# Performance work log

Measured on AMD Instinct MI355X. Metric: run time of the kernel, lower is better.

Reference implementation:

```python
import jax, jax.numpy as jnp
import numpy as np

REEIG_EPS = 1e-4  # SPDNet ReEig eigenvalue floor


def _semi_orth(key, ni, no):
    a = jax.random.normal(key, (ni, no), dtype=jnp.float32)
    q, _ = jnp.linalg.qr(a)  # columns orthonormal (ni >= no)
    return q[None]  # (1, ni, no)


def setup_inputs() -> dict:
    key = jax.random.key(0)
    ks = jax.random.split(key, 6)
    N, C, T, V = 256, 256, 64, 25
    x = jax.random.normal(ks[0], (N, C, T, V), dtype=jnp.float32)
    W1 = _semi_orth(ks[1], 25, 20)
    W2 = _semi_orth(ks[2], 20, 15)
    W3 = _semi_orth(ks[3], 15, 10)
    fc_w = jax.random.normal(ks[4], (64, 100), dtype=jnp.float32) * (1.0 / np.sqrt(100))
    fc_b = jax.random.normal(ks[5], (64,), dtype=jnp.float32) * 0.01
    return {"x": x, "W1": W1, "W2": W2, "W3": W3, "fc_w": fc_w, "fc_b": fc_b}


def _bimap(X, W):
    # X: (n, h, ni, ni), W: (h, ni, no) -> W^T X W : (n, h, no, no)
    return jnp.einsum('hji,nhjk,hkl->nhil', W, X, W)


def _reeig(X):
    w, u = jnp.linalg.eigh(X)
    w = jnp.maximum(w, REEIG_EPS)
    return jnp.einsum('...ij,...j,...kj->...ik', u, w, u)


def _logeig(X):
    w, u = jnp.linalg.eigh(X)
    return jnp.einsum('...ij,...j,...kj->...ik', u, jnp.log(w), u)


def reference(x, W1, W2, W3, fc_w, fc_b):
    N, C, T, V = x.shape
    xm = x.mean(axis=2)                      # (N, C, V): mean over time
    d = xm - xm.mean(axis=1, keepdims=True)  # center over channel samples
    cov = jnp.einsum('ncv,ncw->nvw', d, d) / (C - 1)  # (N, V, V), fused reduction
    cov = cov + jnp.float32(1e-8) * jnp.eye(V, dtype=x.dtype)
    X = cov[:, None, :, :]                   # (N, 1, V, V)
    X = _reeig(_bimap(X, W1))                # 25 -> 20
    X = _reeig(_bimap(X, W2))                # 20 -> 15
    X = _logeig(_reeig(_bimap(X, W3)))       # 15 -> 10, matrix log
    feat = X.reshape(N, -1)                  # (N, 100)
    return feat @ fc_w.T + fc_b              # (N, 64)
```

## Files before the change

kernel.cpp:

```cpp
#include <hip/hip_runtime.h>
#include <math.h>


__device__ __constant__ int d_pairs[9][5][2] = {
    {{9,0},{1,8},{2,7},{3,6},{4,5}},
    {{9,1},{2,0},{3,8},{4,7},{5,6}},
    {{9,2},{3,1},{4,0},{5,8},{6,7}},
    {{9,3},{4,2},{5,1},{6,0},{7,8}},
    {{9,4},{5,3},{6,2},{7,1},{8,0}},
    {{9,5},{6,4},{7,3},{8,2},{0,1}},
    {{9,6},{7,5},{8,4},{0,3},{1,2}},
    {{9,7},{8,6},{0,5},{1,4},{2,3}},
    {{9,8},{0,7},{1,6},{2,5},{3,4}},
};

__global__ __launch_bounds__(1024) void topo_kernel(
    const float* __restrict__ x,
    const float* __restrict__ W1,
    const float* __restrict__ W2,
    const float* __restrict__ W3,
    const float* __restrict__ fcw,
    const float* __restrict__ fcb,
    float* __restrict__ out)
{
    __shared__ float s_xm[6400];
    __shared__ float s_mean[32];
    __shared__ float s_w1[500];
    __shared__ float s_w2[300];
    __shared__ float s_w3[152];
    __shared__ float s_t1[375];
    __shared__ float s_wc[250];
    __shared__ float s_E[2560];
    __shared__ float s_A[100];
    __shared__ float s_U[100];
    __shared__ float s_cp[10], s_cq[10];
    __shared__ int   s_ip[10], s_iq[10];
    __shared__ float s_lw[16];
    __shared__ float s_Y[100];
    __shared__ float s_fcw[100 * 65];

    const int tid = threadIdx.x;
    const int n = blockIdx.x;
    const float* xb = x + (size_t)n * (256 * 64 * 25);

    for (int g = tid; g < 6400; g += 1024) {
        int o = g / 100, k = g - o * 100;
        s_fcw[k * 65 + o] = fcw[g];
    }
    for (int g = tid; g < 500; g += 1024) s_w1[g] = W1[g];
    for (int g = tid; g < 300; g += 1024) s_w2[g] = W2[g];
    if (tid < 150) s_w3[tid] = W3[tid];
    for (int g = tid; g < 6400; g += 1024) s_xm[g] = 0.0f;
    __syncthreads();

    {
        const float4* xb4 = reinterpret_cast<const float4*>(xb);
        for (int task = tid; task < 6400; task += 1024) {
            int c = task / 25;
            int m = task - c * 25;
            const float4* p = xb4 + c * 400 + m;
            float s0 = 0.0f, s1 = 0.0f, s2 = 0.0f, s3 = 0.0f;
#pragma unroll
            for (int k = 0; k < 16; ++k) {
                float4 vv = p[25 * k];
                s0 += vv.x; s1 += vv.y; s2 += vv.z; s3 += vv.w;
            }
            int v = (4 * m) % 25;
            int base = c * 25;
            atomicAdd(&s_xm[base + v], s0); v = (v + 1 == 25) ? 0 : v + 1;
            atomicAdd(&s_xm[base + v], s1); v = (v + 1 == 25) ? 0 : v + 1;
            atomicAdd(&s_xm[base + v], s2); v = (v + 1 == 25) ? 0 : v + 1;
            atomicAdd(&s_xm[base + v], s3);
        }
    }
    __syncthreads();

    for (int g = tid; g < 375; g += 1024) {
        int i = g / 15, l = g - i * 15;
        float s = 0.0f;
#pragma unroll
        for (int j = 0; j < 20; ++j) s += s_w1[i * 20 + j] * s_w2[j * 15 + l];
        s_t1[g] = s;
    }
    if (tid < 25) {
        float s = 0.0f;
        for (int c = 0; c < 256; ++c) s += s_xm[c * 25 + tid];
        s_mean[tid] = s * (1.0f / (64.0f * 256.0f));
    }
    __syncthreads();

    for (int g = tid; g < 250; g += 1024) {
        int i = g / 10, m = g - i * 10;
        float s = 0.0f;
#pragma unroll
        for (int l = 0; l < 15; ++l) s += s_t1[i * 15 + l] * s_w3[l * 10 + m];
        s_wc[g] = s;
    }
    for (int o = tid; o < 6400; o += 1024) {
        int v = o - (o / 25) * 25;
        s_xm[o] = s_xm[o] * (1.0f / 64.0f) - s_mean[v];
    }
    __syncthreads();

    for (int idx = tid; idx < 2560; idx += 1024) {
        int c = idx / 10, i = idx - (idx / 10) * 10;
        float s = 0.0f;
#pragma unroll
        for (int v = 0; v < 25; ++v) s += s_xm[c * 25 + v] * s_wc[v * 10 + i];
        s_E[idx] = s;
    }
    __syncthreads();

    if (tid < 55) {
        int i = 0, rem = tid;
        while (rem >= 10 - i) { rem -= 10 - i; ++i; }
        int j = i + rem;
        float s = 0.0f;
        for (int c = 0; c < 256; ++c) s += s_E[c * 10 + i] * s_E[c * 10 + j];
        float wt = 0.0f;
#pragma unroll
        for (int v = 0; v < 25; ++v) wt += s_wc[v * 10 + i] * s_wc[v * 10 + j];
        float m = s * (1.0f / 255.0f) + 1e-8f * wt;
        s_A[i * 10 + j] = m;
        s_A[j * 10 + i] = m;
    }
    if (tid >= 64 && tid < 164) {
        int e = tid - 64;
        s_U[e] = ((e / 10) == (e % 10)) ? 1.0f : 0.0f;
    }
    __syncthreads();

    for (int sweep = 0; sweep < 8; ++sweep) {
        for (int r = 0; r < 9; ++r) {
            if (tid < 5) {
                int p = d_pairs[r][tid][0], q = d_pairs[r][tid][1];
                if (p > q) { int t = p; p = q; q = t; }
                float app = s_A[p * 10 + p];
                float aqq = s_A[q * 10 + q];
                float apq = s_A[p * 10 + q];
                float c, sn;
                if (fabsf(apq) < 1e-28f) {
                    c = 1.0f; sn = 0.0f;
                } else {
                    float tau = (aqq - app) / (2.0f * apq);
                    float tt = 1.0f / (fabsf(tau) + sqrtf(tau * tau + 1.0f));
                    if (tau < 0.0f) tt = -tt;
                    c = 1.0f / sqrtf(tt * tt + 1.0f);
                    sn = tt * c;
                }
                s_ip[p] = p; s_iq[p] = q; s_cp[p] = c;  s_cq[p] = -sn;
                s_ip[q] = p; s_iq[q] = q; s_cp[q] = sn; s_cq[q] = c;
            }
            __syncthreads();
            float newA = 0.0f, newU = 0.0f;
            if (tid < 100) {
                int i = tid / 10, j = tid - (tid / 10) * 10;
                float wip = s_cp[i], wiq = s_cq[i];
                float wjp = s_cp[j], wjq = s_cq[j];
                int pi_ = s_ip[i], qi_ = s_iq[i];
                int pj  = s_ip[j], qj  = s_iq[j];
                newA = wip * (wjp * s_A[pi_ * 10 + pj] + wjq * s_A[pi_ * 10 + qj])
                     + wiq * (wjp * s_A[qi_ * 10 + pj] + wjq * s_A[qi_ * 10 + qj]);
            } else if (tid < 200) {
                int e = tid - 100;
                int i = e / 10, j = e - (e / 10) * 10;
                int pj = s_ip[j], qj = s_iq[j];
                newU = s_cp[j] * s_U[i * 10 + pj] + s_cq[j] * s_U[i * 10 + qj];
            }
            __syncthreads();
            if (tid < 100)      s_A[tid] = newA;
            else if (tid < 200) s_U[tid - 100] = newU;
            __syncthreads();
        }
    }

    if (tid < 10) s_lw[tid] = logf(fmaxf(s_A[tid * 10 + tid], 1e-4f));
    __syncthreads();

    if (tid < 100) {
        int i = tid / 10, j = tid - (tid / 10) * 10;
        float s = 0.0f;
#pragma unroll
        for (int k = 0; k < 10; ++k) s += s_U[i * 10 + k] * s_lw[k] * s_U[j * 10 + k];
        s_Y[tid] = s;
    }
    __syncthreads();

    if (tid < 64) {
        float s = fcb[tid];
#pragma unroll 4
        for (int k = 0; k < 100; ++k) s += s_Y[k] * s_fcw[k * 65 + tid];
        out[(size_t)n * 64 + tid] = s;
    }
}

extern "C" void kernel_launch(void* const* d_in, const int* in_sizes, int n_in,
                              void* d_out, int out_size, void* d_ws, size_t ws_size,
                              hipStream_t stream) {
    const float* x   = (const float*)d_in[0];
    const float* W1  = (const float*)d_in[1];
    const float* W2  = (const float*)d_in[2];
    const float* W3  = (const float*)d_in[3];
    const float* fcw = (const float*)d_in[4];
    const float* fcb = (const float*)d_in[5];
    float* out = (float*)d_out;

    topo_kernel<<<256, 1024, 0, stream>>>(x, W1, W2, W3, fcw, fcb, out);
}
```

Measured before the change: 604.2 us.

## Split fused kernel into streaming reduction, covariance, and eigen kernels

Replaces the single 256-block kernel with three kernels. A 2048-block time-sum kernel streams the 419 MB input with much more parallelism than the one-block-per-sample design. Covariance and the bilinear projection run in a 256-thread kernel, and the Jacobi eigen/log/FC step runs in a 64-thread kernel, so fewer threads sit idle through the serial sweeps. This costs two extra launches and a workspace round-trip, and keeps the old fused kernel as a fallback when no workspace is available.

```diff
diff --git a/kernel.cpp b/kernel.cpp
--- a/kernel.cpp
+++ b/kernel.cpp
@@ -14,14 +14,43 @@
     {{9,8},{0,7},{1,6},{2,5},{3,4}},
 };
 
-__global__ __launch_bounds__(1024) void topo_kernel(
-    const float* __restrict__ x,
-    const float* __restrict__ W1,
-    const float* __restrict__ W2,
-    const float* __restrict__ W3,
-    const float* __restrict__ fcw,
-    const float* __restrict__ fcb,
-    float* __restrict__ out)
+__global__ __launch_bounds__(256) void k_tsum(
+    const float* __restrict__ x, float* __restrict__ xsum)
+{
+    __shared__ float s_sum[800];
+    const int tid = threadIdx.x;
+    const size_t row0 = (size_t)blockIdx.x * 32;
+
+    for (int g = tid; g < 800; g += 256) s_sum[g] = 0.0f;
+    __syncthreads();
+
+    const float4* base = reinterpret_cast<const float4*>(x) + row0 * 400;
+    for (int task = tid; task < 800; task += 256) {
+        int r = task / 25, m = task - r * 25;
+        const float4* p = base + r * 400 + m;
+        float s0 = 0.0f, s1 = 0.0f, s2 = 0.0f, s3 = 0.0f;
+#pragma unroll
+        for (int k = 0; k < 16; ++k) {
+            float4 vv = p[25 * k];
+            s0 += vv.x; s1 += vv.y; s2 += vv.z; s3 += vv.w;
+        }
+        int v = (4 * m) % 25;
+        int b = r * 25;
+        atomicAdd(&s_sum[b + v], s0); v = (v + 1 == 25) ? 0 : v + 1;
+        atomicAdd(&s_sum[b + v], s1); v = (v + 1 == 25) ? 0 : v + 1;
+        atomicAdd(&s_sum[b + v], s2); v = (v + 1 == 25) ? 0 : v + 1;
+        atomicAdd(&s_sum[b + v], s3);
+    }
+    __syncthreads();
+
+    float* o = xsum + row0 * 25;
+    for (int g = tid; g < 800; g += 256) o[g] = s_sum[g];
+}
+
+__global__ __launch_bounds__(256) void k_cov(
+    const float* __restrict__ xsum,
+    const float* __restrict__ W1, const float* __restrict__ W2,
+    const float* __restrict__ W3, float* __restrict__ Mout)
 {
     __shared__ float s_xm[6400];
     __shared__ float s_mean[32];
@@ -32,6 +61,77 @@
     __shared__ float s_wc[250];
     __shared__ float s_E[2560];
     __shared__ float s_A[100];
+
+    const int tid = threadIdx.x;
+    const int n = blockIdx.x;
+    const float4* xs4 = reinterpret_cast<const float4*>(xsum + (size_t)n * 6400);
+    float4* sm4 = reinterpret_cast<float4*>(s_xm);
+    for (int g = tid; g < 1600; g += 256) sm4[g] = xs4[g];
+    for (int g = tid; g < 500; g += 256) s_w1[g] = W1[g];
+    for (int g = tid; g < 300; g += 256) s_w2[g] = W2[g];
+    if (tid < 150) s_w3[tid] = W3[tid];
+    __syncthreads();
+
+    for (int g = tid; g < 375; g += 256) {
+        int i = g / 15, l = g - i * 15;
+        float s = 0.0f;
+#pragma unroll
+        for (int j = 0; j < 20; ++j) s += s_w1[i * 20 + j] * s_w2[j * 15 + l];
+        s_t1[g] = s;
+    }
+    if (tid < 25) {
+        float s = 0.0f;
+        for (int c = 0; c < 256; ++c) s += s_xm[c * 25 + tid];
+        s_mean[tid] = s * (1.0f / (64.0f * 256.0f));
+    }
+    __syncthreads();
+
+    for (int g = tid; g < 250; g += 256) {
+        int i = g / 10, m = g - i * 10;
+        float s = 0.0f;
+#pragma unroll
+        for (int l = 0; l < 15; ++l) s += s_t1[i * 15 + l] * s_w3[l * 10 + m];
+        s_wc[g] = s;
+    }
+    __syncthreads();
+    for (int o = tid; o < 6400; o += 256) {
+        int v = o - (o / 25) * 25;
+        s_xm[o] = s_xm[o] * (1.0f / 64.0f) - s_mean[v];
+    }
+    __syncthreads();
+
+    for (int idx = tid; idx < 2560; idx += 256) {
+        int c = idx / 10, i = idx - (idx / 10) * 10;
+        float s = 0.0f;
+#pragma unroll
+        for (int v = 0; v < 25; ++v) s += s_xm[c * 25 + v] * s_wc[v * 10 + i];
+        s_E[idx] = s;
+    }
+    __syncthreads();
+
+    if (tid < 55) {
+        int i = 0, rem = tid;
+        while (rem >= 10 - i) { rem -= 10 - i; ++i; }
+        int j = i + rem;
+        float s = 0.0f;
+        for (int c = 0; c < 256; ++c) s += s_E[c * 10 + i] * s_E[c * 10 + j];
+        float wt = 0.0f;
+#pragma unroll
+        for (int v = 0; v < 25; ++v) wt += s_wc[v * 10 + i] * s_wc[v * 10 + j];
+        float m = s * (1.0f / 255.0f) + 1e-8f * wt;
+        s_A[i * 10 + j] = m;
+        s_A[j * 10 + i] = m;
+    }
+    __syncthreads();
+    if (tid < 100) Mout[(size_t)n * 100 + tid] = s_A[tid];
+}
+
+__global__ __launch_bounds__(64) void k_eig(
+    const float* __restrict__ Min,
+    const float* __restrict__ fcw, const float* __restrict__ fcb,
+    float* __restrict__ out)
+{
+    __shared__ float s_A[100];
     __shared__ float s_U[100];
     __shared__ float s_cp[10], s_cq[10];
     __shared__ int   s_ip[10], s_iq[10];
@@ -41,91 +141,24 @@
 
     const int tid = threadIdx.x;
     const int n = blockIdx.x;
-    const float* xb = x + (size_t)n * (256 * 64 * 25);
-
-    for (int g = tid; g < 6400; g += 1024) {
-        int o = g / 100, k = g - o * 100;
-        s_fcw[k * 65 + o] = fcw[g];
-    }
-    for (int g = tid; g < 500; g += 1024) s_w1[g] = W1[g];
-    for (int g = tid; g < 300; g += 1024) s_w2[g] = W2[g];
-    if (tid < 150) s_w3[tid] = W3[tid];
-    for (int g = tid; g < 6400; g += 1024) s_xm[g] = 0.0f;
-    __syncthreads();
 
     {
-        const float4* xb4 = reinterpret_cast<const float4*>(xb);
-        for (int task = tid; task < 6400; task += 1024) {
-            int c = task / 25;
-            int m = task - c * 25;
-            const float4* p = xb4 + c * 400 + m;
-            float s0 = 0.0f, s1 = 0.0f, s2 = 0.0f, s3 = 0.0f;
-#pragma unroll
-            for (int k = 0; k < 16; ++k) {
-                float4 vv = p[25 * k];
-                s0 += vv.x; s1 += vv.y; s2 += vv.z; s3 += vv.w;
-            }
-            int v = (4 * m) % 25;
-            int base = c * 25;
-            atomicAdd(&s_xm[base + v], s0); v = (v + 1 == 25) ? 0 : v + 1;
-            atomicAdd(&s_xm[base + v], s1); v = (v + 1 == 25) ? 0 : v + 1;
-            atomicAdd(&s_xm[base + v], s2); v = (v + 1 == 25) ? 0 : v + 1;
-            atomicAdd(&s_xm[base + v], s3);
+        const float4* fw4 = reinterpret_cast<const float4*>(fcw);
+        for (int g4 = tid; g4 < 1600; g4 += 64) {
+            float4 w = fw4[g4];
+            int o = g4 / 25, k4 = (g4 - o * 25) * 4;
+            s_fcw[(k4 + 0) * 65 + o] = w.x;
+            s_fcw[(k4 + 1) * 65 + o] = w.y;
+            s_fcw[(k4 + 2) * 65 + o] = w.z;
+            s_fcw[(k4 + 3) * 65 + o] = w.w;
         }
     }
-    __syncthreads();
-
-    for (int g = tid; g < 375; g += 1024) {
-        int i = g / 15, l = g - i * 15;
-        float s = 0.0f;
-#pragma unroll
-        for (int j = 0; j < 20; ++j) s += s_w1[i * 20 + j] * s_w2[j * 15 + l];
-        s_t1[g] = s;
-    }
-    if (tid < 25) {
-        float s = 0.0f;
-        for (int c = 0; c < 256; ++c) s += s_xm[c * 25 + tid];
-        s_mean[tid] = s * (1.0f / (64.0f * 256.0f));
-    }
-    __syncthreads();
-
-    for (int g = tid; g < 250; g += 1024) {
-        int i = g / 10, m = g - i * 10;
-        float s = 0.0f;
-#pragma unroll
-        for (int l = 0; l < 15; ++l) s += s_t1[i * 15 + l] * s_w3[l * 10 + m];
-        s_wc[g] = s;
-    }
-    for (int o = tid; o < 6400; o += 1024) {
-        int v = o - (o / 25) * 25;
-        s_xm[o] = s_xm[o] * (1.0f / 64.0f) - s_mean[v];
-    }
-    __syncthreads();
-
-    for (int idx = tid; idx < 2560; idx += 1024) {
-        int c = idx / 10, i = idx - (idx / 10) * 10;
-        float s = 0.0f;
-#pragma unroll
-        for (int v = 0; v < 25; ++v) s += s_xm[c * 25 + v] * s_wc[v * 10 + i];
-        s_E[idx] = s;
-    }
-    __syncthreads();
-
-    if (tid < 55) {
-        int i = 0, rem = tid;
-        while (rem >= 10 - i) { rem -= 10 - i; ++i; }
-        int j = i + rem;
-        float s = 0.0f;
-        for (int c = 0; c < 256; ++c) s += s_E[c * 10 + i] * s_E[c * 10 + j];
-        float wt = 0.0f;
-#pragma unroll
-        for (int v = 0; v < 25; ++v) wt += s_wc[v * 10 + i] * s_wc[v * 10 + j];
-        float m = s * (1.0f / 255.0f) + 1e-8f * wt;
-        s_A[i * 10 + j] = m;
-        s_A[j * 10 + i] = m;
-    }
-    if (tid >= 64 && tid < 164) {
-        int e = tid - 64;
+    const float* Mn = Min + (size_t)n * 100;
+    s_A[tid] = Mn[tid];
+    if (tid < 36) s_A[tid + 64] = Mn[tid + 64];
+    s_U[tid] = ((tid / 10) == (tid % 10)) ? 1.0f : 0.0f;
+    if (tid < 36) {
+        int e = tid + 64;
         s_U[e] = ((e / 10) == (e % 10)) ? 1.0f : 0.0f;
     }
     __syncthreads();
@@ -152,6 +185,200 @@
                 s_ip[q] = p; s_iq[q] = q; s_cp[q] = sn; s_cq[q] = c;
             }
             __syncthreads();
+
+            float nA0, nU0, nA1 = 0.0f, nU1 = 0.0f;
+            {
+                int e = tid;
+                int i = e / 10, j = e - (e / 10) * 10;
+                float wip = s_cp[i], wiq = s_cq[i];
+                float wjp = s_cp[j], wjq = s_cq[j];
+                int pi_ = s_ip[i], qi_ = s_iq[i];
+                int pj  = s_ip[j], qj  = s_iq[j];
+                nA0 = wip * (wjp * s_A[pi_ * 10 + pj] + wjq * s_A[pi_ * 10 + qj])
+                    + wiq * (wjp * s_A[qi_ * 10 + pj] + wjq * s_A[qi_ * 10 + qj]);
+                nU0 = wjp * s_U[i * 10 + pj] + wjq * s_U[i * 10 + qj];
+            }
+            if (tid < 36) {
+                int e = tid + 64;
+                int i = e / 10, j = e - (e / 10) * 10;
+                float wip = s_cp[i], wiq = s_cq[i];
+                float wjp = s_cp[j], wjq = s_cq[j];
+                int pi_ = s_ip[i], qi_ = s_iq[i];
+                int pj  = s_ip[j], qj  = s_iq[j];
+                nA1 = wip * (wjp * s_A[pi_ * 10 + pj] + wjq * s_A[pi_ * 10 + qj])
+                    + wiq * (wjp * s_A[qi_ * 10 + pj] + wjq * s_A[qi_ * 10 + qj]);
+                nU1 = wjp * s_U[i * 10 + pj] + wjq * s_U[i * 10 + qj];
+            }
+            __syncthreads();
+            s_A[tid] = nA0; s_U[tid] = nU0;
+            if (tid < 36) { s_A[tid + 64] = nA1; s_U[tid + 64] = nU1; }
+            __syncthreads();
+        }
+    }
+
+    if (tid < 10) s_lw[tid] = logf(fmaxf(s_A[tid * 11], 1e-4f));
+    __syncthreads();
+
+    {
+        int i = tid / 10, j = tid - (tid / 10) * 10;
+        float s = 0.0f;
+#pragma unroll
+        for (int k = 0; k < 10; ++k) s += s_U[i * 10 + k] * s_lw[k] * s_U[j * 10 + k];
+        s_Y[tid] = s;
+    }
+    if (tid < 36) {
+        int e = tid + 64;
+        int i = e / 10, j = e - (e / 10) * 10;
+        float s = 0.0f;
+#pragma unroll
+        for (int k = 0; k < 10; ++k) s += s_U[i * 10 + k] * s_lw[k] * s_U[j * 10 + k];
+        s_Y[e] = s;
+    }
+    __syncthreads();
+
+    {
+        float s = fcb[tid];
+#pragma unroll 4
+        for (int k = 0; k < 100; ++k) s += s_Y[k] * s_fcw[k * 65 + tid];
+        out[(size_t)n * 64 + tid] = s;
+    }
+}
+
+__global__ __launch_bounds__(1024) void topo_fused(
+    const float* __restrict__ x, const float* __restrict__ W1,
+    const float* __restrict__ W2, const float* __restrict__ W3,
+    const float* __restrict__ fcw, const float* __restrict__ fcb,
+    float* __restrict__ out)
+{
+    __shared__ float s_xm[6400];
+    __shared__ float s_mean[32];
+    __shared__ float s_w1[500];
+    __shared__ float s_w2[300];
+    __shared__ float s_w3[152];
+    __shared__ float s_t1[375];
+    __shared__ float s_wc[250];
+    __shared__ float s_E[2560];
+    __shared__ float s_A[100];
+    __shared__ float s_U[100];
+    __shared__ float s_cp[10], s_cq[10];
+    __shared__ int   s_ip[10], s_iq[10];
+    __shared__ float s_lw[16];
+    __shared__ float s_Y[100];
+    __shared__ float s_fcw[100 * 65];
+
+    const int tid = threadIdx.x;
+    const int n = blockIdx.x;
+    const float* xb = x + (size_t)n * (256 * 64 * 25);
+
+    for (int g = tid; g < 6400; g += 1024) {
+        int o = g / 100, k = g - o * 100;
+        s_fcw[k * 65 + o] = fcw[g];
+    }
+    for (int g = tid; g < 500; g += 1024) s_w1[g] = W1[g];
+    for (int g = tid; g < 300; g += 1024) s_w2[g] = W2[g];
+    if (tid < 150) s_w3[tid] = W3[tid];
+    for (int g = tid; g < 6400; g += 1024) s_xm[g] = 0.0f;
+    __syncthreads();
+
+    {
+        const float4* xb4 = reinterpret_cast<const float4*>(xb);
+        for (int task = tid; task < 6400; task += 1024) {
+            int c = task / 25;
+            int m = task - c * 25;
+            const float4* p = xb4 + c * 400 + m;
+            float s0 = 0.0f, s1 = 0.0f, s2 = 0.0f, s3 = 0.0f;
+#pragma unroll
+            for (int k = 0; k < 16; ++k) {
+                float4 vv = p[25 * k];
+                s0 += vv.x; s1 += vv.y; s2 += vv.z; s3 += vv.w;
+            }
+            int v = (4 * m) % 25;
+            int base = c * 25;
+            atomicAdd(&s_xm[base + v], s0); v = (v + 1 == 25) ? 0 : v + 1;
+            atomicAdd(&s_xm[base + v], s1); v = (v + 1 == 25) ? 0 : v + 1;
+            atomicAdd(&s_xm[base + v], s2); v = (v + 1 == 25) ? 0 : v + 1;
+            atomicAdd(&s_xm[base + v], s3);
+        }
+    }
+    __syncthreads();
+
+    for (int g = tid; g < 375; g += 1024) {
+        int i = g / 15, l = g - i * 15;
+        float s = 0.0f;
+#pragma unroll
+        for (int j = 0; j < 20; ++j) s += s_w1[i * 20 + j] * s_w2[j * 15 + l];
+        s_t1[g] = s;
+    }
+    if (tid < 25) {
+        float s = 0.0f;
+        for (int c = 0; c < 256; ++c) s += s_xm[c * 25 + tid];
+        s_mean[tid] = s * (1.0f / (64.0f * 256.0f));
+    }
+    __syncthreads();
+
+    for (int g = tid; g < 250; g += 1024) {
+        int i = g / 10, m = g - i * 10;
+        float s = 0.0f;
+#pragma unroll
+        for (int l = 0; l < 15; ++l) s += s_t1[i * 15 + l] * s_w3[l * 10 + m];
+        s_wc[g] = s;
+    }
+    for (int o = tid; o < 6400; o += 1024) {
+        int v = o - (o / 25) * 25;
+        s_xm[o] = s_xm[o] * (1.0f / 64.0f) - s_mean[v];
+    }
+    __syncthreads();
+
+    for (int idx = tid; idx < 2560; idx += 1024) {
+        int c = idx / 10, i = idx - (idx / 10) * 10;
+        float s = 0.0f;
+#pragma unroll
+        for (int v = 0; v < 25; ++v) s += s_xm[c * 25 + v] * s_wc[v * 10 + i];
+        s_E[idx] = s;
+    }
+    __syncthreads();
+
+    if (tid < 55) {
+        int i = 0, rem = tid;
+        while (rem >= 10 - i) { rem -= 10 - i; ++i; }
+        int j = i + rem;
+        float s = 0.0f;
+        for (int c = 0; c < 256; ++c) s += s_E[c * 10 + i] * s_E[c * 10 + j];
+        float wt = 0.0f;
+#pragma unroll
+        for (int v = 0; v < 25; ++v) wt += s_wc[v * 10 + i] * s_wc[v * 10 + j];
+        float m = s * (1.0f / 255.0f) + 1e-8f * wt;
+        s_A[i * 10 + j] = m;
+        s_A[j * 10 + i] = m;
+    }
+    if (tid >= 64 && tid < 164) {
+        int e = tid - 64;
+        s_U[e] = ((e / 10) == (e % 10)) ? 1.0f : 0.0f;
+    }
+    __syncthreads();
+
+    for (int sweep = 0; sweep < 8; ++sweep) {
+        for (int r = 0; r < 9; ++r) {
+            if (tid < 5) {
+                int p = d_pairs[r][tid][0], q = d_pairs[r][tid][1];
+                if (p > q) { int t = p; p = q; q = t; }
+                float app = s_A[p * 10 + p];
+                float aqq = s_A[q * 10 + q];
+                float apq = s_A[p * 10 + q];
+                float c, sn;
+                if (fabsf(apq) < 1e-28f) {
+                    c = 1.0f; sn = 0.0f;
+                } else {
+                    float tau = (aqq - app) / (2.0f * apq);
+                    float tt = 1.0f / (fabsf(tau) + sqrtf(tau * tau + 1.0f));
+                    if (tau < 0.0f) tt = -tt;
+                    c = 1.0f / sqrtf(tt * tt + 1.0f);
+                    sn = tt * c;
+                }
+                s_ip[p] = p; s_iq[p] = q; s_cp[p] = c;  s_cq[p] = -sn;
+                s_ip[q] = p; s_iq[q] = q; s_cp[q] = sn; s_cq[q] = c;
+            }
+            __syncthreads();
             float newA = 0.0f, newU = 0.0f;
             if (tid < 100) {
                 int i = tid / 10, j = tid - (tid / 10) * 10;
@@ -205,5 +432,16 @@
     const float* fcb = (const float*)d_in[5];
     float* out = (float*)d_out;
 
-    topo_kernel<<<256, 1024, 0, stream>>>(x, W1, W2, W3, fcw, fcb, out);
+    const size_t XSUM_FLOATS = (size_t)65536 * 25;
+    const size_t NEED = (XSUM_FLOATS + 256 * 100) * sizeof(float);
+
+    if (d_ws != nullptr && ws_size >= NEED) {
+        float* xsum = (float*)d_ws;
+        float* M    = xsum + XSUM_FLOATS;
+        k_tsum<<<2048, 256, 0, stream>>>(x, xsum);
+        k_cov <<<256, 256, 0, stream>>>(xsum, W1, W2, W3, M);
+        k_eig <<<256, 64, 0, stream>>>(M, fcw, fcb, out);
+    } else {
+        topo_fused<<<256, 1024, 0, stream>>>(x, W1, W2, W3, fcw, fcb, out);
+    }
 }
```

Result: slower. 616.8 us (+2.1%).
